# Kernel tuning notes

Hardware: AMD Instinct MI355X
Metric: run time of the kernel (lower is better)

Reference implementation:

```python
import jax, jax.numpy as jnp
import numpy as np

B, T, D, H = 2, 2048, 1024, 16
HD = D // H            # head dim = 64
WINDOW = 512           # sliding-window size
EPS = 1e-6
ROPE_BASE = 10000.0


def setup_inputs() -> dict:
    key = jax.random.key(0)
    ks = jax.random.split(key, 5)
    s = 0.02  # init scale for dense kernels
    return {
        "x": jax.random.normal(ks[0], (B, T, D), jnp.float32),
        "Wq": jax.random.normal(ks[1], (D, D), jnp.float32) * s,
        "Wk": jax.random.normal(ks[2], (D, D), jnp.float32) * s,
        "Wv": jax.random.normal(ks[3], (D, D), jnp.float32) * s,
        "Wo": jax.random.normal(ks[4], (D, D), jnp.float32) * s,
        "q_scale": jnp.ones((HD,), jnp.float32),
        "k_scale": jnp.ones((HD,), jnp.float32),
        "sink_logit": jnp.zeros((H,), jnp.float32),
    }


def _rmsnorm(x, scale):
    # x: [..., HD]
    var = jnp.mean(jnp.square(x), axis=-1, keepdims=True)
    return x * jax.lax.rsqrt(var + EPS) * scale


def _rope(x):
    # x: [B, H, T, HD]; standard rotate-half RoPE over the full head dim
    half = HD // 2
    inv_freq = 1.0 / (ROPE_BASE ** (jnp.arange(0, HD, 2, dtype=jnp.float32) / HD))  # [half]
    t = jnp.arange(T, dtype=jnp.float32)
    freqs = t[:, None] * inv_freq[None, :]                # [T, half]
    emb = jnp.concatenate([freqs, freqs], axis=-1)        # [T, HD]
    cos = jnp.cos(emb)[None, None]                        # [1,1,T,HD]
    sin = jnp.sin(emb)[None, None]
    x1, x2 = x[..., :half], x[..., half:]
    rot = jnp.concatenate([-x2, x1], axis=-1)
    return x * cos + rot * sin


def reference(x, Wq, Wk, Wv, Wo, q_scale, k_scale, sink_logit):
    # projections -> [B, T, H, HD]
    q = (x @ Wq).reshape(B, T, H, HD)
    k = (x @ Wk).reshape(B, T, H, HD)
    v = (x @ Wv).reshape(B, T, H, HD)
    # QK RMSNorm over head dim
    q = _rmsnorm(q, q_scale)
    k = _rmsnorm(k, k_scale)
    # -> [B, H, T, HD], then RoPE
    q = _rope(q.transpose(0, 2, 1, 3))
    k = _rope(k.transpose(0, 2, 1, 3))
    v = v.transpose(0, 2, 1, 3)
    # causal sliding-window mask
    idx = jnp.arange(T)
    rel = idx[None, :] - idx[:, None]                     # key - query
    mask = ((rel <= 0) & (rel > -WINDOW))[None, None]     # [1,1,T,T]
    scale = HD ** (-0.5)
    scores = jnp.einsum('bhtd,bhsd->bhts', q, k) * scale
    scores = jnp.where(mask, scores, -jnp.inf)
    # sink-augmented softmax: append per-head sink logit to denominator
    sink = jnp.broadcast_to(sink_logit.reshape(1, H, 1, 1), (B, H, T, 1))
    aug = jnp.concatenate([scores.astype(jnp.float32), sink.astype(jnp.float32)], axis=-1)
    weights = jax.nn.softmax(aug, axis=-1)[..., :T].astype(scores.dtype)
    out = jnp.einsum('bhts,bhsd->bhtd', weights, v)
    out = out.transpose(0, 2, 1, 3).reshape(B, T, D)
    return out @ Wo
```

## Files before the change

kernel.cpp:

```cpp
#include <hip/hip_runtime.h>
#include <math.h>

#define CB 2
#define CT 2048
#define CD 1024
#define CH 16
#define CHD 64
#define CWINDOW 512

typedef __bf16 bf16x8 __attribute__((ext_vector_type(8)));
typedef float floatx4 __attribute__((ext_vector_type(4)));

__device__ __forceinline__ unsigned short f2bf(float f) {
  union { float f; unsigned int u; } v;
  v.f = f;
  unsigned int u = v.u;
  u += 0x7fffu + ((u >> 16) & 1u);
  return (unsigned short)(u >> 16);
}
__device__ __forceinline__ unsigned short f2bf_trunc(float f) {
  union { float f; unsigned int u; } v;
  v.f = f;
  return (unsigned short)(v.u >> 16);
}
__device__ __forceinline__ float bf2f(unsigned int h) {
  union { unsigned int u; float f; } v;
  v.u = h << 16;
  return v.f;
}

__global__ __launch_bounds__(256) void cvt_all(const float* __restrict__ x,
                                               const float* __restrict__ Wq,
                                               const float* __restrict__ Wk,
                                               const float* __restrict__ Wv,
                                               const float* __restrict__ Wo,
                                               unsigned short* __restrict__ xb,
                                               unsigned short* __restrict__ WqT,
                                               unsigned short* __restrict__ WkT,
                                               unsigned short* __restrict__ WvT,
                                               unsigned short* __restrict__ WoT) {
  const int z = blockIdx.z;
  if (z < 4) {
    const float* W = z == 0 ? Wq : z == 1 ? Wk : z == 2 ? Wv : Wo;
    unsigned short* Wt = z == 0 ? WqT : z == 1 ? WkT : z == 2 ? WvT : WoT;
    __shared__ float tile[64][65];
    const int k0 = blockIdx.x * 64, n0 = blockIdx.y * 64;
    const int c = threadIdx.x & 63, r4 = threadIdx.x >> 6;
#pragma unroll
    for (int i = 0; i < 16; ++i) {
      int r = i * 4 + r4;
      tile[r][c] = W[(size_t)(k0 + r) * CD + n0 + c];
    }
    __syncthreads();
#pragma unroll
    for (int i = 0; i < 16; ++i) {
      int r = i * 4 + r4;
      Wt[(size_t)(n0 + r) * CD + k0 + c] = f2bf(tile[c][r]);
    }
  } else {
    const int idx = (z - 4) * 256 + blockIdx.y * 16 + blockIdx.x;
    const int i = idx * 256 + threadIdx.x;
    float4 a = ((const float4*)x)[i * 2];
    float4 b = ((const float4*)x)[i * 2 + 1];
    uint4 o;
    o.x = (unsigned int)f2bf(a.x) | ((unsigned int)f2bf(a.y) << 16);
    o.y = (unsigned int)f2bf(a.z) | ((unsigned int)f2bf(a.w) << 16);
    o.z = (unsigned int)f2bf(b.x) | ((unsigned int)f2bf(b.y) << 16);
    o.w = (unsigned int)f2bf(b.z) | ((unsigned int)f2bf(b.w) << 16);
    ((uint4*)xb)[i] = o;
  }
}

__device__ __forceinline__ void async16(const unsigned short* g, unsigned short* l) {
  __builtin_amdgcn_global_load_lds(
      (const __attribute__((address_space(1))) unsigned int*)g,
      (__attribute__((address_space(3))) unsigned int*)l, 16, 0, 0);
}

template <int MODE, int BM>
__device__ __forceinline__ void mfma_gemm_body(const unsigned short* __restrict__ A,
                                               const unsigned short* __restrict__ Bt,
                                               void* __restrict__ Cout,
                                               const float* __restrict__ scale,
                                               float oscale) {
  constexpr int K = CD;
  constexpr int MT = BM / 32;
  __shared__ unsigned short As[BM * 32];
  __shared__ unsigned short Bs[128 * 32];
  const int tid = threadIdx.x;
  const int wave = tid >> 6, lane = tid & 63;
  const int m0 = blockIdx.x * BM, n0 = blockIdx.y * 128;
  const int mq = (wave & 1) * (BM / 2), nq = (wave >> 1) * 64;

  floatx4 acc[MT][4] = {};
  const int srow = lane >> 2;
  const int skc = (lane & 3) * 8;
  const int fr = lane & 15;
  const int fk = (lane >> 4) * 8;

  for (int k0 = 0; k0 < K; k0 += 32) {
    __syncthreads();
#pragma unroll
    for (int it = 0; it < BM / 64; ++it) {
      const int sub = wave * (BM / 64) + it;
      const int row = sub * 16 + srow;
      async16(A + (size_t)(m0 + row) * K + k0 + skc, &As[sub * 512]);
    }
#pragma unroll
    for (int it = 0; it < 2; ++it) {
      const int sub = wave * 2 + it;
      const int row = sub * 16 + srow;
      async16(Bt + (size_t)(n0 + row) * K + k0 + skc, &Bs[sub * 512]);
    }
    __syncthreads();
    bf16x8 af[MT], bg[4];
#pragma unroll
    for (int mt = 0; mt < MT; ++mt)
      af[mt] = *(const bf16x8*)&As[(mq + mt * 16 + fr) * 32 + fk];
#pragma unroll
    for (int nt = 0; nt < 4; ++nt)
      bg[nt] = *(const bf16x8*)&Bs[(nq + nt * 16 + fr) * 32 + fk];
#pragma unroll
    for (int mt = 0; mt < MT; ++mt)
#pragma unroll
      for (int nt = 0; nt < 4; ++nt)
        acc[mt][nt] = __builtin_amdgcn_mfma_f32_16x16x32_bf16(af[mt], bg[nt], acc[mt][nt], 0, 0, 0);
  }

  if (MODE == 1) {
    const int c = lane & 15;
    const int g = lane >> 4;
    const int hh = (n0 + nq) >> 6;
    const float kf = -0.2878231366242557f;
    const float inv0 = __expf((float)c * kf);
    const float inv1 = __expf((float)(16 + c) * kf);
    float sc[4];
#pragma unroll
    for (int nt = 0; nt < 4; ++nt) sc[nt] = scale[nt * 16 + c];
#pragma unroll
    for (int mt = 0; mt < MT; ++mt) {
#pragma unroll
      for (int i = 0; i < 4; ++i) {
        const int m = m0 + mq + mt * 16 + g * 4 + i;
        const int b = m >> 11, t = m & (CT - 1);
        float v0 = acc[mt][0][i], v1 = acc[mt][1][i];
        float v2 = acc[mt][2][i], v3 = acc[mt][3][i];
        float ss = v0 * v0 + v1 * v1 + v2 * v2 + v3 * v3;
#pragma unroll
        for (int off = 8; off > 0; off >>= 1) ss += __shfl_xor(ss, off);
        const float rs = rsqrtf(ss * (1.0f / 64.0f) + 1e-6f);
        v0 *= rs * sc[0];
        v1 *= rs * sc[1];
        v2 *= rs * sc[2];
        v3 *= rs * sc[3];
        const float tf = (float)t;
        const float a0 = tf * inv0, a1 = tf * inv1;
        const float s0 = __sinf(a0), c0 = __cosf(a0);
        const float s1 = __sinf(a1), c1 = __cosf(a1);
        unsigned short* dst = (unsigned short*)Cout + ((size_t)(b * CH + hh) * CT + t) * CHD;
        ushort4 o;
        o.x = f2bf((v0 * c0 - v2 * s0) * oscale);
        o.y = f2bf((v1 * c1 - v3 * s1) * oscale);
        o.z = f2bf((v2 * c0 + v0 * s0) * oscale);
        o.w = f2bf((v3 * c1 + v1 * s1) * oscale);
        *(ushort4*)&dst[4 * c] = o;
      }
    }
  } else {
#pragma unroll
    for (int mt = 0; mt < MT; ++mt) {
#pragma unroll
      for (int nt = 0; nt < 4; ++nt) {
        const int col = n0 + nq + nt * 16 + (lane & 15);
        if (MODE == 2) {
          const int mb = m0 + mq + mt * 16 + (lane >> 4) * 4;
          const int b = mb >> 11, t = mb & (CT - 1);
          const int h = col >> 6, d = col & 63;
          ushort4 o;
          o.x = f2bf(acc[mt][nt][0]);
          o.y = f2bf(acc[mt][nt][1]);
          o.z = f2bf(acc[mt][nt][2]);
          o.w = f2bf(acc[mt][nt][3]);
          *(ushort4*)&((unsigned short*)Cout)[((size_t)(b * CH + h) * CHD + d) * CT + t] = o;
        } else {
#pragma unroll
          for (int i = 0; i < 4; ++i) {
            const int m = m0 + mq + mt * 16 + (lane >> 4) * 4 + i;
            ((float*)Cout)[(size_t)m * CD + col] = acc[mt][nt][i];
          }
        }
      }
    }
  }
}

__global__ __launch_bounds__(256, 3) void gemm_qkv_mfma(const unsigned short* __restrict__ xb,
                                                        const unsigned short* __restrict__ WqT,
                                                        const unsigned short* __restrict__ WkT,
                                                        const unsigned short* __restrict__ WvT,
                                                        unsigned short* __restrict__ Qh,
                                                        unsigned short* __restrict__ Kh,
                                                        unsigned short* __restrict__ Vt,
                                                        const float* __restrict__ q_scale,
                                                        const float* __restrict__ k_scale) {
  if (blockIdx.z == 2) {
    mfma_gemm_body<2, 128>(xb, WvT, Vt, nullptr, 1.0f);
  } else if (blockIdx.z == 0) {
    mfma_gemm_body<1, 128>(xb, WqT, Qh, q_scale, 0.125f);
  } else {
    mfma_gemm_body<1, 128>(xb, WkT, Kh, k_scale, 1.0f);
  }
}

__global__ __launch_bounds__(256, 3) void gemm_out_mfma(const unsigned short* __restrict__ AO,
                                                        const unsigned short* __restrict__ WoT,
                                                        float* __restrict__ out) {
  mfma_gemm_body<0, 64>(AO, WoT, out, nullptr, 1.0f);
}

__device__ __forceinline__ bf16x8 frag64(const unsigned short* base, int row, int ks, int lane) {
  const int phys = (((ks << 2) + (lane >> 4)) ^ (lane & 7)) << 3;
  return *(const bf16x8*)&base[(row << 6) + phys];
}

__global__ __launch_bounds__(256, 3) void attn_mfma(const unsigned short* __restrict__ Qh,
                                                    const unsigned short* __restrict__ Kh,
                                                    const unsigned short* __restrict__ Vt,
                                                    const float* __restrict__ sink_logit,
                                                    unsigned short* __restrict__ AO) {
  __shared__ unsigned short Qs[128 * 64];
  __shared__ unsigned short Ks[64 * 64];
  __shared__ unsigned short Vs[64 * 64];
  __shared__ unsigned short Ps[128 * 72];

  const int tid = threadIdx.x;
  const int w = tid >> 6, lane = tid & 63;
  const int qb = blockIdx.x, bh = blockIdx.y;
  const int b = bh >> 4, h = bh & 15;
  const int q0 = qb * 128;
  const unsigned short* Qb = Qh + (size_t)bh * CT * CHD;
  const unsigned short* Kb = Kh + (size_t)bh * CT * CHD;
  const unsigned short* Vb = Vt + (size_t)bh * CHD * CT;

  const int l7 = lane & 7, l8 = lane >> 3;
  const int sx8 = (l7 ^ l8) * 8;

#pragma unroll
  for (int s = 0; s < 4; ++s) {
    const int slab = w * 4 + s;
    async16(Qb + (size_t)(q0 + slab * 8 + l8) * CHD + sx8, &Qs[slab * 512]);
  }
  __syncthreads();
  bf16x8 qf[2][2];
#pragma unroll
  for (int nt = 0; nt < 2; ++nt)
#pragma unroll
    for (int ks = 0; ks < 2; ++ks)
      qf[nt][ks] = frag64(Qs, w * 32 + nt * 16 + (lane & 15), ks, lane);

  floatx4 acc[4][2] = {};
  float lsum[2] = {0.f, 0.f};
  const int qw = q0 + w * 32;

  const int kb_lo = (qb >= 4) ? (qb * 2 - 8) : 0;
  const int kb_hi = qb * 2 + 1;
  for (int kb = kb_lo; kb <= kb_hi; ++kb) {
    __syncthreads();
#pragma unroll
    for (int s = 0; s < 2; ++s) {
      const int slab = w * 2 + s;
      const int row = slab * 8 + l8;
      async16(Kb + (size_t)(kb * 64 + row) * CHD + sx8, &Ks[slab * 512]);
      async16(Vb + (size_t)row * CT + kb * 64 + sx8, &Vs[slab * 512]);
    }
    __syncthreads();

    const int kmin = kb * 64, kmax = kb * 64 + 63;
    if (kmin > qw + 31 || kmax <= qw - CWINDOW) continue;

    floatx4 st[4][2] = {};
#pragma unroll
    for (int ks = 0; ks < 2; ++ks) {
      bf16x8 kf[4];
#pragma unroll
      for (int mt = 0; mt < 4; ++mt)
        kf[mt] = frag64(Ks, mt * 16 + (lane & 15), ks, lane);
#pragma unroll
      for (int mt = 0; mt < 4; ++mt)
#pragma unroll
        for (int nt = 0; nt < 2; ++nt)
          st[mt][nt] = __builtin_amdgcn_mfma_f32_16x16x32_bf16(kf[mt], qf[nt][ks], st[mt][nt], 0, 0, 0);
    }

    const bool need_c = (kmax > qw);
    const bool need_w = (kmin <= qw + 31 - CWINDOW);
#pragma unroll
    for (int mt = 0; mt < 4; ++mt) {
#pragma unroll
      for (int nt = 0; nt < 2; ++nt) {
        const int s_base = kb * 64 + mt * 16 + (lane >> 4) * 4;
        const int t_g = q0 + w * 32 + nt * 16 + (lane & 15);
        ushort4 pk;
        float psum = 0.f;
#pragma unroll
        for (int i = 0; i < 4; ++i) {
          float sv = st[mt][nt][i];
          if (need_c || need_w) {
            const int s_g = s_base + i;
            const bool ok = (!need_c || (s_g <= t_g)) && (!need_w || (s_g > t_g - CWINDOW));
            sv = ok ? sv : -INFINITY;
          }
          const unsigned short pb = f2bf_trunc(__expf(sv));
          ((unsigned short*)&pk)[i] = pb;
          psum += bf2f(pb);
        }
        lsum[nt] += psum;
        const int qrow = w * 32 + nt * 16 + (lane & 15);
        const int scol = mt * 16 + (lane >> 4) * 4;
        *(ushort4*)&Ps[qrow * 72 + scol] = pk;
      }
    }

#pragma unroll
    for (int ks = 0; ks < 2; ++ks) {
      bf16x8 vf[4], pf[2];
#pragma unroll
      for (int mt = 0; mt < 4; ++mt)
        vf[mt] = frag64(Vs, mt * 16 + (lane & 15), ks, lane);
#pragma unroll
      for (int nt = 0; nt < 2; ++nt) {
        const int qrow = w * 32 + nt * 16 + (lane & 15);
        pf[nt] = *(const bf16x8*)&Ps[qrow * 72 + ks * 32 + (lane >> 4) * 8];
      }
#pragma unroll
      for (int mt = 0; mt < 4; ++mt)
#pragma unroll
        for (int nt = 0; nt < 2; ++nt)
          acc[mt][nt] = __builtin_amdgcn_mfma_f32_16x16x32_bf16(vf[mt], pf[nt], acc[mt][nt], 0, 0, 0);
    }
  }

  const float sinkw = __expf(sink_logit[h]);
  float inv[2];
#pragma unroll
  for (int nt = 0; nt < 2; ++nt) {
    float l = lsum[nt];
    l += __shfl_xor(l, 16);
    l += __shfl_xor(l, 32);
    inv[nt] = 1.0f / (l + sinkw);
  }
#pragma unroll
  for (int mt = 0; mt < 4; ++mt) {
#pragma unroll
    for (int nt = 0; nt < 2; ++nt) {
      const int t_g = q0 + w * 32 + nt * 16 + (lane & 15);
      const int d0 = mt * 16 + (lane >> 4) * 4;
      ushort4 o;
      o.x = f2bf(acc[mt][nt][0] * inv[nt]);
      o.y = f2bf(acc[mt][nt][1] * inv[nt]);
      o.z = f2bf(acc[mt][nt][2] * inv[nt]);
      o.w = f2bf(acc[mt][nt][3] * inv[nt]);
      *(ushort4*)&AO[(size_t)(b * CT + t_g) * CD + h * CHD + d0] = o;
    }
  }
}

extern "C" void kernel_launch(void* const* d_in, const int* in_sizes, int n_in,
                              void* d_out, int out_size, void* d_ws, size_t ws_size,
                              hipStream_t stream) {
  (void)in_sizes;
  (void)n_in;
  (void)out_size;
  (void)ws_size;
  const float* x = (const float*)d_in[0];
  const float* Wq = (const float*)d_in[1];
  const float* Wk = (const float*)d_in[2];
  const float* Wv = (const float*)d_in[3];
  const float* Wo = (const float*)d_in[4];
  const float* q_scale = (const float*)d_in[5];
  const float* k_scale = (const float*)d_in[6];
  const float* sink = (const float*)d_in[7];
  float* out = (float*)d_out;

  const size_t per = (size_t)CB * CH * CT * CHD;
  unsigned short* Qh = (unsigned short*)d_ws;
  unsigned short* Kh = Qh + per;
  unsigned short* Vt = Kh + per;
  unsigned short* AO = Vt + per;
  unsigned short* xb = AO + per;
  unsigned short* WqT = xb + per;
  unsigned short* WkT = WqT + (size_t)CD * CD;
  unsigned short* WvT = WkT + (size_t)CD * CD;
  unsigned short* WoT = WvT + (size_t)CD * CD;

  dim3 blk(256);
  cvt_all<<<dim3(16, 16, 12), blk, 0, stream>>>(x, Wq, Wk, Wv, Wo, xb, WqT, WkT, WvT, WoT);
  gemm_qkv_mfma<<<dim3(32, 8, 3), blk, 0, stream>>>(xb, WqT, WkT, WvT, Qh, Kh, Vt, q_scale, k_scale);
  attn_mfma<<<dim3(CT / 128, CB * CH), blk, 0, stream>>>(Qh, Kh, Vt, sink, AO);
  gemm_out_mfma<<<dim3(64, 8), blk, 0, stream>>>(AO, WoT, out);
}
```

Measured before the change: 166.3 us.

## Fuse Q/K/V projections into one GEMM kernel sharing the x tile

Replaces the three-way blockIdx.z dispatch of separate Q, K and V GEMMs (128-row tiles, 768 blocks) with one kernel that loads a 64-row x tile once and multiplies it against all three weight tiles, keeping three accumulator sets per wave. This cuts redundant global loads of x and gives more MFMA work per A fragment. In exchange the grid shrinks to 512 blocks, register pressure rises (occupancy target lowered to 2) and B-tile LDS traffic per iteration triples. The output GEMM is split out into its own standalone kernel with the same 64-row tiling as before.

```diff
diff --git a/kernel.cpp b/kernel.cpp
--- a/kernel.cpp
+++ b/kernel.cpp
@@ -77,74 +77,84 @@
       (__attribute__((address_space(3))) unsigned int*)l, 16, 0, 0);
 }
 
-template <int MODE, int BM>
-__device__ __forceinline__ void mfma_gemm_body(const unsigned short* __restrict__ A,
-                                               const unsigned short* __restrict__ Bt,
-                                               void* __restrict__ Cout,
-                                               const float* __restrict__ scale,
-                                               float oscale) {
+__global__ __launch_bounds__(256, 2) void gemm_qkv_fused(const unsigned short* __restrict__ xb,
+                                                         const unsigned short* __restrict__ WqT,
+                                                         const unsigned short* __restrict__ WkT,
+                                                         const unsigned short* __restrict__ WvT,
+                                                         unsigned short* __restrict__ Qh,
+                                                         unsigned short* __restrict__ Kh,
+                                                         unsigned short* __restrict__ Vt,
+                                                         const float* __restrict__ q_scale,
+                                                         const float* __restrict__ k_scale) {
   constexpr int K = CD;
-  constexpr int MT = BM / 32;
-  __shared__ unsigned short As[BM * 32];
-  __shared__ unsigned short Bs[128 * 32];
+  __shared__ unsigned short As[64 * 32];
+  __shared__ unsigned short Bs[3][128 * 32];
   const int tid = threadIdx.x;
   const int wave = tid >> 6, lane = tid & 63;
-  const int m0 = blockIdx.x * BM, n0 = blockIdx.y * 128;
-  const int mq = (wave & 1) * (BM / 2), nq = (wave >> 1) * 64;
-
-  floatx4 acc[MT][4] = {};
+  const int m0 = blockIdx.x * 64, n0 = blockIdx.y * 128;
+  const int mq = (wave & 1) * 32, nq = (wave >> 1) * 64;
+
+  floatx4 acc[3][2][4] = {};
   const int srow = lane >> 2;
   const int skc = (lane & 3) * 8;
   const int fr = lane & 15;
   const int fk = (lane >> 4) * 8;
 
+  const unsigned short* Wt[3] = {WqT, WkT, WvT};
+
   for (int k0 = 0; k0 < K; k0 += 32) {
     __syncthreads();
-#pragma unroll
-    for (int it = 0; it < BM / 64; ++it) {
-      const int sub = wave * (BM / 64) + it;
-      const int row = sub * 16 + srow;
-      async16(A + (size_t)(m0 + row) * K + k0 + skc, &As[sub * 512]);
-    }
-#pragma unroll
-    for (int it = 0; it < 2; ++it) {
-      const int sub = wave * 2 + it;
-      const int row = sub * 16 + srow;
-      async16(Bt + (size_t)(n0 + row) * K + k0 + skc, &Bs[sub * 512]);
-    }
-    __syncthreads();
-    bf16x8 af[MT], bg[4];
-#pragma unroll
-    for (int mt = 0; mt < MT; ++mt)
+    async16(xb + (size_t)(m0 + wave * 16 + srow) * K + k0 + skc, &As[wave * 512]);
+#pragma unroll
+    for (int j = 0; j < 3; ++j) {
+#pragma unroll
+      for (int it = 0; it < 2; ++it) {
+        const int sub = wave * 2 + it;
+        async16(Wt[j] + (size_t)(n0 + sub * 16 + srow) * K + k0 + skc, &Bs[j][sub * 512]);
+      }
+    }
+    __syncthreads();
+    bf16x8 af[2];
+#pragma unroll
+    for (int mt = 0; mt < 2; ++mt)
       af[mt] = *(const bf16x8*)&As[(mq + mt * 16 + fr) * 32 + fk];
 #pragma unroll
-    for (int nt = 0; nt < 4; ++nt)
-      bg[nt] = *(const bf16x8*)&Bs[(nq + nt * 16 + fr) * 32 + fk];
-#pragma unroll
-    for (int mt = 0; mt < MT; ++mt)
+    for (int j = 0; j < 3; ++j) {
+      bf16x8 bg[4];
 #pragma unroll
       for (int nt = 0; nt < 4; ++nt)
-        acc[mt][nt] = __builtin_amdgcn_mfma_f32_16x16x32_bf16(af[mt], bg[nt], acc[mt][nt], 0, 0, 0);
-  }
-
-  if (MODE == 1) {
-    const int c = lane & 15;
-    const int g = lane >> 4;
-    const int hh = (n0 + nq) >> 6;
-    const float kf = -0.2878231366242557f;
-    const float inv0 = __expf((float)c * kf);
-    const float inv1 = __expf((float)(16 + c) * kf);
+        bg[nt] = *(const bf16x8*)&Bs[j][(nq + nt * 16 + fr) * 32 + fk];
+#pragma unroll
+      for (int mt = 0; mt < 2; ++mt)
+#pragma unroll
+        for (int nt = 0; nt < 4; ++nt)
+          acc[j][mt][nt] = __builtin_amdgcn_mfma_f32_16x16x32_bf16(af[mt], bg[nt], acc[j][mt][nt], 0, 0, 0);
+    }
+  }
+
+  const int c = lane & 15;
+  const int g = lane >> 4;
+  const int hh = (n0 + nq) >> 6;
+  const float kf = -0.2878231366242557f;
+  const float inv0 = __expf((float)c * kf);
+  const float inv1 = __expf((float)(16 + c) * kf);
+
+#pragma unroll
+  for (int j = 0; j < 2; ++j) {
+    const float* scale = (j == 0) ? q_scale : k_scale;
+    unsigned short* Co = (j == 0) ? Qh : Kh;
+    const float oscale = (j == 0) ? 0.125f : 1.0f;
     float sc[4];
 #pragma unroll
     for (int nt = 0; nt < 4; ++nt) sc[nt] = scale[nt * 16 + c];
 #pragma unroll
-    for (int mt = 0; mt < MT; ++mt) {
+    for (int mt = 0; mt < 2; ++mt) {
 #pragma unroll
       for (int i = 0; i < 4; ++i) {
         const int m = m0 + mq + mt * 16 + g * 4 + i;
         const int b = m >> 11, t = m & (CT - 1);
-        float v0 = acc[mt][0][i], v1 = acc[mt][1][i];
-        float v2 = acc[mt][2][i], v3 = acc[mt][3][i];
+        float v0 = acc[j][mt][0][i], v1 = acc[j][mt][1][i];
+        float v2 = acc[j][mt][2][i], v3 = acc[j][mt][3][i];
         float ss = v0 * v0 + v1 * v1 + v2 * v2 + v3 * v3;
 #pragma unroll
         for (int off = 8; off > 0; off >>= 1) ss += __shfl_xor(ss, off);
@@ -157,7 +167,7 @@
         const float a0 = tf * inv0, a1 = tf * inv1;
         const float s0 = __sinf(a0), c0 = __cosf(a0);
         const float s1 = __sinf(a1), c1 = __cosf(a1);
-        unsigned short* dst = (unsigned short*)Cout + ((size_t)(b * CH + hh) * CT + t) * CHD;
+        unsigned short* dst = Co + ((size_t)(b * CH + hh) * CT + t) * CHD;
         ushort4 o;
         o.x = f2bf((v0 * c0 - v2 * s0) * oscale);
         o.y = f2bf((v1 * c1 - v3 * s1) * oscale);
@@ -166,56 +176,78 @@
         *(ushort4*)&dst[4 * c] = o;
       }
     }
-  } else {
-#pragma unroll
-    for (int mt = 0; mt < MT; ++mt) {
-#pragma unroll
-      for (int nt = 0; nt < 4; ++nt) {
-        const int col = n0 + nq + nt * 16 + (lane & 15);
-        if (MODE == 2) {
-          const int mb = m0 + mq + mt * 16 + (lane >> 4) * 4;
-          const int b = mb >> 11, t = mb & (CT - 1);
-          const int h = col >> 6, d = col & 63;
-          ushort4 o;
-          o.x = f2bf(acc[mt][nt][0]);
-          o.y = f2bf(acc[mt][nt][1]);
-          o.z = f2bf(acc[mt][nt][2]);
-          o.w = f2bf(acc[mt][nt][3]);
-          *(ushort4*)&((unsigned short*)Cout)[((size_t)(b * CH + h) * CHD + d) * CT + t] = o;
-        } else {
-#pragma unroll
-          for (int i = 0; i < 4; ++i) {
-            const int m = m0 + mq + mt * 16 + (lane >> 4) * 4 + i;
-            ((float*)Cout)[(size_t)m * CD + col] = acc[mt][nt][i];
-          }
-        }
+  }
+
+#pragma unroll
+  for (int mt = 0; mt < 2; ++mt) {
+#pragma unroll
+    for (int nt = 0; nt < 4; ++nt) {
+      const int col = n0 + nq + nt * 16 + c;
+      const int mb = m0 + mq + mt * 16 + g * 4;
+      const int b = mb >> 11, t = mb & (CT - 1);
+      const int h = col >> 6, d = col & 63;
+      ushort4 o;
+      o.x = f2bf(acc[2][mt][nt][0]);
+      o.y = f2bf(acc[2][mt][nt][1]);
+      o.z = f2bf(acc[2][mt][nt][2]);
+      o.w = f2bf(acc[2][mt][nt][3]);
+      *(ushort4*)&Vt[((size_t)(b * CH + h) * CHD + d) * CT + t] = o;
+    }
+  }
+}
+
+__global__ __launch_bounds__(256, 3) void gemm_out_mfma(const unsigned short* __restrict__ A,
+                                                        const unsigned short* __restrict__ Bt,
+                                                        float* __restrict__ Cout) {
+  constexpr int K = CD;
+  __shared__ unsigned short As[64 * 32];
+  __shared__ unsigned short Bs[128 * 32];
+  const int tid = threadIdx.x;
+  const int wave = tid >> 6, lane = tid & 63;
+  const int m0 = blockIdx.x * 64, n0 = blockIdx.y * 128;
+  const int mq = (wave & 1) * 32, nq = (wave >> 1) * 64;
+
+  floatx4 acc[2][4] = {};
+  const int srow = lane >> 2;
+  const int skc = (lane & 3) * 8;
+  const int fr = lane & 15;
+  const int fk = (lane >> 4) * 8;
+
+  for (int k0 = 0; k0 < K; k0 += 32) {
+    __syncthreads();
+    async16(A + (size_t)(m0 + wave * 16 + srow) * K + k0 + skc, &As[wave * 512]);
+#pragma unroll
+    for (int it = 0; it < 2; ++it) {
+      const int sub = wave * 2 + it;
+      async16(Bt + (size_t)(n0 + sub * 16 + srow) * K + k0 + skc, &Bs[sub * 512]);
+    }
+    __syncthreads();
+    bf16x8 af[2], bg[4];
+#pragma unroll
+    for (int mt = 0; mt < 2; ++mt)
+      af[mt] = *(const bf16x8*)&As[(mq + mt * 16 + fr) * 32 + fk];
+#pragma unroll
+    for (int nt = 0; nt < 4; ++nt)
+      bg[nt] = *(const bf16x8*)&Bs[(nq + nt * 16 + fr) * 32 + fk];
+#pragma unroll
+    for (int mt = 0; mt < 2; ++mt)
+#pragma unroll
+      for (int nt = 0; nt < 4; ++nt)
+        acc[mt][nt] = __builtin_amdgcn_mfma_f32_16x16x32_bf16(af[mt], bg[nt], acc[mt][nt], 0, 0, 0);
+  }
+
+#pragma unroll
+  for (int mt = 0; mt < 2; ++mt) {
+#pragma unroll
+    for (int nt = 0; nt < 4; ++nt) {
+      const int col = n0 + nq + nt * 16 + (lane & 15);
+#pragma unroll
+      for (int i = 0; i < 4; ++i) {
+        const int m = m0 + mq + mt * 16 + (lane >> 4) * 4 + i;
+        Cout[(size_t)m * CD + col] = acc[mt][nt][i];
       }
     }
   }
-}
-
-__global__ __launch_bounds__(256, 3) void gemm_qkv_mfma(const unsigned short* __restrict__ xb,
-                                                        const unsigned short* __restrict__ WqT,
-                                                        const unsigned short* __restrict__ WkT,
-                                                        const unsigned short* __restrict__ WvT,
-                                                        unsigned short* __restrict__ Qh,
-                                                        unsigned short* __restrict__ Kh,
-                                                        unsigned short* __restrict__ Vt,
-                                                        const float* __restrict__ q_scale,
-                                                        const float* __restrict__ k_scale) {
-  if (blockIdx.z == 2) {
-    mfma_gemm_body<2, 128>(xb, WvT, Vt, nullptr, 1.0f);
-  } else if (blockIdx.z == 0) {
-    mfma_gemm_body<1, 128>(xb, WqT, Qh, q_scale, 0.125f);
-  } else {
-    mfma_gemm_body<1, 128>(xb, WkT, Kh, k_scale, 1.0f);
-  }
-}
-
-__global__ __launch_bounds__(256, 3) void gemm_out_mfma(const unsigned short* __restrict__ AO,
-                                                        const unsigned short* __restrict__ WoT,
-                                                        float* __restrict__ out) {
-  mfma_gemm_body<0, 64>(AO, WoT, out, nullptr, 1.0f);
 }
 
 __device__ __forceinline__ bf16x8 frag64(const unsigned short* base, int row, int ks, int lane) {
@@ -395,7 +427,7 @@
 
   dim3 blk(256);
   cvt_all<<<dim3(16, 16, 12), blk, 0, stream>>>(x, Wq, Wk, Wv, Wo, xb, WqT, WkT, WvT, WoT);
-  gemm_qkv_mfma<<<dim3(32, 8, 3), blk, 0, stream>>>(xb, WqT, WkT, WvT, Qh, Kh, Vt, q_scale, k_scale);
+  gemm_qkv_fused<<<dim3(64, 8), blk, 0, stream>>>(xb, WqT, WkT, WvT, Qh, Kh, Vt, q_scale, k_scale);
   attn_mfma<<<dim3(CT / 128, CB * CH), blk, 0, stream>>>(Qh, Kh, Vt, sink, AO);
   gemm_out_mfma<<<dim3(64, 8), blk, 0, stream>>>(AO, WoT, out);
 }
```

New measurement: 177.6 us. 6.8% more time.
